# Optimization experiments

Measured on AMD Instinct MI355X. Metric: run time of the kernel, lower is better.

## Reference

```python
import jax, jax.numpy as jnp
import numpy as np

B, S, IN_DIM, OUT_DIM = 4, 2048, 1024, 1024
NEG = -9e15

def _xavier(key, shape, gain=1.414):
    fan_in, fan_out = shape[0], shape[1]
    a = gain * np.sqrt(6.0 / (fan_in + fan_out))
    return jax.random.uniform(key, shape, jnp.float32, -a, a)

def setup_inputs() -> dict:
    key = jax.random.key(0)
    ks = jax.random.split(key, 8)
    x = jax.random.normal(ks[0], (B, S, IN_DIM), jnp.float32)
    W_query = _xavier(ks[1], (IN_DIM, OUT_DIM))
    W_key = _xavier(ks[2], (IN_DIM, OUT_DIM))
    W_value = _xavier(ks[3], (IN_DIM, OUT_DIM))
    # torch Linear default init (kaiming-uniform-ish); values don't matter for correctness baseline
    W1 = _xavier(ks[4], (OUT_DIM + IN_DIM, OUT_DIM), gain=1.0)
    b1 = jnp.zeros((OUT_DIM,), jnp.float32)
    W2 = _xavier(ks[5], (OUT_DIM, OUT_DIM), gain=1.0)
    b2 = jnp.zeros((OUT_DIM,), jnp.float32)
    return {"x": x, "W_query": W_query, "W_key": W_key, "W_value": W_value,
            "W1": W1, "b1": b1, "W2": W2, "b2": b2}

def reference(x, W_query, W_key, W_value, W1, b1, W2, b2):
    # QKV projections: [B,S,in] @ [in,out] -> [B,S,out]
    q = jnp.einsum('bsi,io->bso', x, W_query)
    k = jnp.einsum('bsi,io->bso', x, W_key)
    v = jnp.einsum('bsi,io->bso', x, W_value)
    scale = 1.0 / jnp.sqrt(jnp.float32(OUT_DIM))
    e = jnp.einsum('bqd,bkd->bqk', q, k) * scale  # [B,S,S]
    causal = jnp.tril(jnp.ones((S, S), jnp.float32))  # mask > 0 keeps lower triangle
    attn = jnp.where(causal > 0, e, jnp.float32(NEG))
    attn = jax.nn.softmax(attn, axis=2)
    # dropout: eval mode (train=False) -> identity
    out = jnp.einsum('bqk,bkd->bqd', attn, v)  # [B,S,out]
    h = jnp.concatenate([out, x], axis=-1)  # [B,S,out+in]
    h = jax.nn.relu(jnp.einsum('bsf,fo->bso', h, W1) + b1)
    return jnp.einsum('bsf,fo->bso', h, W2) + b2
```

## Files before the change

kernel.cpp:

```cpp
#include <hip/hip_runtime.h>
#include <stdint.h>

typedef __attribute__((ext_vector_type(8))) short short8;
typedef __attribute__((ext_vector_type(4))) float f32x4;

__device__ __forceinline__ unsigned short f32_to_bf16(float f) {
    unsigned int u = __float_as_uint(f);
    u += 0x7FFFu + ((u >> 16) & 1u);
    return (unsigned short)(u >> 16);
}

__device__ __forceinline__ short8 load8_f32_as_bf16(const float* __restrict__ ap) {
    f32x4 f0 = *(const f32x4*)ap;
    f32x4 f1 = *(const f32x4*)(ap + 4);
    union { short8 s; unsigned short u[8]; } cv;
#pragma unroll
    for (int t = 0; t < 4; ++t) {
        cv.u[t]     = f32_to_bf16(f0[t]);
        cv.u[t + 4] = f32_to_bf16(f1[t]);
    }
    return cv.s;
}

__device__ __forceinline__ void gld_lds16(const void* g, void* l) {
    __builtin_amdgcn_global_load_lds(
        (const __attribute__((address_space(1))) unsigned int*)(unsigned long long)(uintptr_t)g,
        (__attribute__((address_space(3))) unsigned int*)(unsigned int)(uintptr_t)l,
        16, 0, 0);
}

template<int AMODE, int EPI, int SWIZ, bool KLIMIT>
__global__ __launch_bounds__(256, 4)
void gemm128(const unsigned short* __restrict__ A, const unsigned short* __restrict__ A2,
             int lda, int lda2, int ksplit,
             const unsigned short* __restrict__ B, int ldb,
             void* __restrict__ C, int ldc, int K,
             long aStride, long bStride, long cStride,
             const float* __restrict__ bias, long biasStride, float scale)
{
    int z = blockIdx.z;
    int mblk, nblk;
    if (SWIZ == 1) {
        int lin = blockIdx.y * gridDim.x + blockIdx.x;
        int mchunk = gridDim.y >> 3;
        int xcd = lin & 7, idx = lin >> 3;
        mblk = xcd * mchunk + idx % mchunk;
        nblk = idx / mchunk;
    } else if (SWIZ == 2) {
        int x = blockIdx.x;
        int a = (int)((sqrtf(8.f * x + 1.f) - 1.f) * 0.5f);
        while ((a + 1) * (a + 2) / 2 <= x) ++a;
        while (a * (a + 1) / 2 > x) --a;
        mblk = a;
        nblk = x - a * (a + 1) / 2;
    } else if (SWIZ == 3) {
        int lin = blockIdx.y * gridDim.x + blockIdx.x;
        int nchunk = gridDim.x >> 3;
        int xcd = lin & 7, idx = lin >> 3;
        nblk = xcd * nchunk + idx % nchunk;
        mblk = idx / nchunk;
    } else if (SWIZ == 4) {
        mblk = (z & 2) ? ((int)gridDim.y - 1 - (int)blockIdx.y) : blockIdx.y;
        nblk = blockIdx.x;
    } else {
        mblk = blockIdx.y;
        nblk = blockIdx.x;
    }
    int m0 = mblk * 128;
    int n0 = nblk * 128;

    const unsigned short* Ab = A + (size_t)z * aStride;
    const unsigned short* Bb = B + (size_t)z * bStride;

    __shared__ __align__(16) short As[128 * 64];
    __shared__ __align__(16) short Bs[128 * 64];

    int tid  = threadIdx.x;
    int lane = tid & 63, wid = tid >> 6;
    int wm = (wid & 1) * 64, wn = (wid >> 1) * 64;
    int fr = lane & 15, fq = lane >> 4;
    int sw0 = ((fq    ) ^ (fr & 7)) * 16;
    int sw1 = ((fq ^ 4) ^ (fr & 7)) * 16;

    int rS = tid >> 3;
    int cS = ((tid & 7) ^ (rS & 7)) * 8;
    char* AsB = (char*)As; char* BsB = (char*)Bs;

    int kend = KLIMIT ? min(K, m0 + 128) : K;

    f32x4 acc[4][4];
#pragma unroll
    for (int i = 0; i < 4; ++i)
#pragma unroll
    for (int j = 0; j < 4; ++j) acc[i][j] = f32x4{0.f, 0.f, 0.f, 0.f};

    for (int k0 = 0; k0 < kend; k0 += 64) {
        const unsigned short* Asrc = Ab;
        int koff = k0, ldax = lda;
        if (AMODE == 2 && k0 >= ksplit) { Asrc = A2; koff = k0 - ksplit; ldax = lda2; }
        const unsigned short* pa = Asrc + (size_t)(m0 + rS) * ldax + koff + cS;
        const unsigned short* pb = Bb   + (size_t)(n0 + rS) * ldb  + k0   + cS;
#pragma unroll
        for (int t = 0; t < 4; ++t) {
            gld_lds16(pa + (size_t)(32 * t) * ldax, AsB + t * 4096 + tid * 16);
            gld_lds16(pb + (size_t)(32 * t) * ldb,  BsB + t * 4096 + tid * 16);
        }
        __syncthreads();

#pragma unroll
        for (int kh = 0; kh < 2; ++kh) {
            int sw = kh ? sw1 : sw0;
            short8 a[4], b[4];
#pragma unroll
            for (int i = 0; i < 4; ++i) {
                a[i] = *(const short8*)(AsB + (wm + i * 16 + fr) * 128 + sw);
                b[i] = *(const short8*)(BsB + (wn + i * 16 + fr) * 128 + sw);
            }
#pragma unroll
            for (int i = 0; i < 4; ++i)
#pragma unroll
            for (int j = 0; j < 4; ++j)
                acc[i][j] = __builtin_amdgcn_mfma_f32_16x16x32_bf16(a[i], b[j], acc[i][j], 0, 0, 0);
        }
        __syncthreads();
    }

    if (EPI == 6) {
        unsigned short* Cz = (unsigned short*)C + (size_t)z * cStride;
        float* rs = const_cast<float*>(bias) + z * biasStride;
#pragma unroll
        for (int i = 0; i < 4; ++i)
#pragma unroll
        for (int r = 0; r < 4; ++r) {
            int row = m0 + wm + i * 16 + fq * 4 + r;
            float s = 0.f;
#pragma unroll
            for (int j = 0; j < 4; ++j) {
                int col = n0 + wn + j * 16 + fr;
                float e = (col <= row) ? __expf(acc[i][j][r] * scale - 16.f) : 0.f;
                s += e;
                Cz[(size_t)row * ldc + col] = f32_to_bf16(e);
            }
            s += __shfl_xor(s, 1);
            s += __shfl_xor(s, 2);
            s += __shfl_xor(s, 4);
            s += __shfl_xor(s, 8);
            if (fr == 0) atomicAdd(&rs[row], s);
        }
    } else if (EPI == 4) {
        unsigned short* Cz = (unsigned short*)C + (size_t)z * cStride;
#pragma unroll
        for (int i = 0; i < 4; ++i)
#pragma unroll
        for (int r = 0; r < 4; ++r) {
            int row = m0 + wm + i * 16 + fq * 4 + r;
            float inv = 1.f / bias[z * biasStride + row];
#pragma unroll
            for (int j = 0; j < 4; ++j) {
                int col = n0 + wn + j * 16 + fr;
                Cz[(size_t)row * ldc + col] = f32_to_bf16(acc[i][j][r] * inv);
            }
        }
    } else {
#pragma unroll
        for (int i = 0; i < 4; ++i)
#pragma unroll
        for (int j = 0; j < 4; ++j)
#pragma unroll
        for (int r = 0; r < 4; ++r) {
            int row = m0 + wm + i * 16 + fq * 4 + r;
            int col = n0 + wn + j * 16 + fr;
            float v = acc[i][j][r];
            if (EPI == 0) {
                ((unsigned short*)C + (size_t)z * cStride)[(size_t)row * ldc + col] = f32_to_bf16(v);
            } else if (EPI == 2) {
                v += bias[col];
                v = v > 0.f ? v : 0.f;
                ((unsigned short*)C + (size_t)z * cStride)[(size_t)row * ldc + col] = f32_to_bf16(v);
            } else {
                ((float*)C + (size_t)z * cStride)[(size_t)row * ldc + col] = v + bias[col];
            }
        }
    }
}

__device__ __forceinline__ void transpose_tile32(const float* __restrict__ in,
                                                 unsigned short* __restrict__ out,
                                                 int rows, int cols, int bx, int by, int tid)
{
    __shared__ float t[32][33];
    int tx = tid & 31, ty = tid >> 5;
    int r0 = by * 32, c0 = bx * 32;
#pragma unroll
    for (int i = 0; i < 4; ++i)
        t[ty + i * 8][tx] = in[(size_t)(r0 + ty + i * 8) * cols + c0 + tx];
    __syncthreads();
#pragma unroll
    for (int i = 0; i < 4; ++i)
        out[(size_t)(c0 + ty + i * 8) * rows + r0 + tx] = f32_to_bf16(t[tx][ty + i * 8]);
}

__global__ __launch_bounds__(256)
void prep_kernel(const float* __restrict__ x,
                 const float* __restrict__ Wq, const float* __restrict__ Wk,
                 const float* __restrict__ Wv, const float* __restrict__ W1,
                 const float* __restrict__ W2,
                 unsigned short* __restrict__ xb, unsigned short* __restrict__ WT,
                 unsigned short* __restrict__ W1T, unsigned short* __restrict__ W2T,
                 float* __restrict__ rsum)
{
    int idx = blockIdx.x;
    int tid = threadIdx.x;
    if (idx < 4096) {
        size_t i = ((size_t)idx * 256 + tid) * 8;
        *(short8*)(xb + i) = load8_f32_as_bf16(x + i);
    } else if (idx < 7168) {
        int t = idx - 4096;
        int w = t >> 10; t &= 1023;
        const float* in = w == 0 ? Wq : (w == 1 ? Wk : Wv);
        transpose_tile32(in, WT + (size_t)w * 1024 * 1024, 1024, 1024,
                         t & 31, t >> 5, tid);
    } else if (idx < 9216) {
        int t = idx - 7168;
        transpose_tile32(W1, W1T, 2048, 1024, t & 31, t >> 5, tid);
    } else if (idx < 10240) {
        int t = idx - 9216;
        transpose_tile32(W2, W2T, 1024, 1024, t & 31, t >> 5, tid);
    } else {
        int t = idx - 10240;
        f32x4 zero = {0.f, 0.f, 0.f, 0.f};
        float* p = rsum + ((size_t)t * 256 + tid) * 8;
        *(f32x4*)p = zero;
        *(f32x4*)(p + 4) = zero;
    }
}

extern "C" void kernel_launch(void* const* d_in, const int* in_sizes, int n_in,
                              void* d_out, int out_size, void* d_ws, size_t ws_size,
                              hipStream_t stream)
{
    const float* x  = (const float*)d_in[0];
    const float* Wq = (const float*)d_in[1];
    const float* Wk = (const float*)d_in[2];
    const float* Wv = (const float*)d_in[3];
    const float* W1 = (const float*)d_in[4];
    const float* b1 = (const float*)d_in[5];
    const float* W2 = (const float*)d_in[6];
    const float* b2 = (const float*)d_in[7];
    float* out = (float*)d_out;

    size_t off = 0;
    auto alloc = [&](size_t bytes) {
        char* r = (char*)d_ws + off;
        off += (bytes + 255) & ~(size_t)255;
        return r;
    };
    const size_t TOK = (size_t)8192 * 1024;
    unsigned short* WT   = (unsigned short*)alloc((size_t)3072 * 1024 * 2);
    unsigned short* W1T  = (unsigned short*)alloc((size_t)1024 * 2048 * 2);
    unsigned short* W2T  = (unsigned short*)alloc((size_t)1024 * 1024 * 2);
    unsigned short* xb   = (unsigned short*)alloc(TOK * 2);
    unsigned short* vT   = (unsigned short*)alloc((size_t)1024 * 8192 * 2);
    unsigned short* attn = (unsigned short*)alloc(TOK * 2);
    float*          rsum = (float*)         alloc((size_t)4 * 2048 * 4);
    unsigned short* q    = (unsigned short*)alloc(TOK * 2);
    unsigned short* k    = (unsigned short*)alloc(TOK * 2);
    unsigned short* S    = (unsigned short*)alloc((size_t)4 * 2048 * 2048 * 2);
    unsigned short* h1   = S;

    prep_kernel<<<10244, 256, 0, stream>>>(x, Wq, Wk, Wv, W1, W2, xb, WT, W1T, W2T, rsum);

    gemm128<0, 0, 1, false><<<dim3(8, 64, 2), 256, 0, stream>>>(
        xb, nullptr, 1024, 0, 0, WT, 1024, q, 1024, 1024,
        0, (long)1024 * 1024, (long)TOK, nullptr, 0, 0.f);
    gemm128<0, 0, 3, false><<<dim3(64, 8, 1), 256, 0, stream>>>(
        WT + (size_t)2 * 1024 * 1024, nullptr, 1024, 0, 0, xb, 1024, vT, 8192, 1024,
        0, 0, 0, nullptr, 0, 0.f);

    gemm128<0, 6, 2, false><<<dim3(136, 1, 4), 256, 0, stream>>>(
        q, nullptr, 1024, 0, 0, k, 1024, S, 2048, 1024,
        (long)2048 * 1024, (long)2048 * 1024, (long)2048 * 2048, rsum, 2048, 0.03125f);
    gemm128<0, 4, 4, true><<<dim3(8, 16, 4), 256, 0, stream>>>(
        S, nullptr, 2048, 0, 0, vT, 8192, attn, 1024, 2048,
        (long)2048 * 2048, (long)2048, (long)2048 * 1024, rsum, 2048, 0.f);

    gemm128<2, 2, 1, false><<<dim3(8, 64, 1), 256, 0, stream>>>(
        attn, xb, 1024, 1024, 1024, W1T, 2048, h1, 1024, 2048, 0, 0, 0, b1, 0, 0.f);
    gemm128<0, 3, 1, false><<<dim3(8, 64, 1), 256, 0, stream>>>(
        h1, nullptr, 1024, 0, 0, W2T, 1024, out, 1024, 1024, 0, 0, 0, b2, 0, 0.f);
}
```

Before: 301.5 us.

## Use 64-row M tiles, fuse QKV launches, add finer causal tile mapping

Adds an M-tile template parameter and switches the attention, MLP and scores GEMMs to 64x128 tiles, which doubles the block count so more CUs are busy and causal skipping becomes finer grained. The q/k and transposed-v projections are merged into a single launch with a z-dependent operand swap and a second output pointer. A new triangular index mapping for 64-row blocks replaces the old 128x128 one. Smaller tiles lower per-block arithmetic intensity and add global load traffic in exchange for better occupancy and load balance.

New measurement: 299.5 us. No clear change (-0.7%).

```diff
diff --git a/kernel.cpp b/kernel.cpp
--- a/kernel.cpp
+++ b/kernel.cpp
@@ -29,14 +29,20 @@
         16, 0, 0);
 }
 
-template<int AMODE, int EPI, int SWIZ, bool KLIMIT>
+__device__ __forceinline__ int triC(int y) {
+    int t = y >> 1;
+    return y + t * (t - 1) + ((y & 1) ? t : 0);
+}
+
+template<int AMODE, int EPI, int SWIZ, bool KLIMIT, int MT>
 __global__ __launch_bounds__(256, 4)
 void gemm128(const unsigned short* __restrict__ A, const unsigned short* __restrict__ A2,
              int lda, int lda2, int ksplit,
              const unsigned short* __restrict__ B, int ldb,
              void* __restrict__ C, int ldc, int K,
              long aStride, long bStride, long cStride,
-             const float* __restrict__ bias, long biasStride, float scale)
+             const float* __restrict__ bias, long biasStride, float scale,
+             void* __restrict__ C2, int ldc2)
 {
     int z = blockIdx.z;
     int mblk, nblk;
@@ -46,38 +52,45 @@
         int xcd = lin & 7, idx = lin >> 3;
         mblk = xcd * mchunk + idx % mchunk;
         nblk = idx / mchunk;
-    } else if (SWIZ == 2) {
-        int x = blockIdx.x;
-        int a = (int)((sqrtf(8.f * x + 1.f) - 1.f) * 0.5f);
-        while ((a + 1) * (a + 2) / 2 <= x) ++a;
-        while (a * (a + 1) / 2 > x) --a;
-        mblk = a;
-        nblk = x - a * (a + 1) / 2;
-    } else if (SWIZ == 3) {
-        int lin = blockIdx.y * gridDim.x + blockIdx.x;
-        int nchunk = gridDim.x >> 3;
-        int xcd = lin & 7, idx = lin >> 3;
-        nblk = xcd * nchunk + idx % nchunk;
-        mblk = idx / nchunk;
     } else if (SWIZ == 4) {
         mblk = (z & 2) ? ((int)gridDim.y - 1 - (int)blockIdx.y) : blockIdx.y;
         nblk = blockIdx.x;
+    } else if (SWIZ == 5) {
+        int x = blockIdx.x;
+        int a = (int)(2.f * sqrtf((float)x));
+        if (a > 31) a = 31;
+        while (a < 31 && triC(a + 1) <= x) ++a;
+        while (a > 0 && triC(a) > x) --a;
+        mblk = a;
+        nblk = x - triC(a);
+    } else if (SWIZ == 6) {
+        int x = blockIdx.x, yy = blockIdx.y;
+        if (z < 2) { mblk = x * 8 + (yy & 7); nblk = yy >> 3; }
+        else       { nblk = x * 8 + (yy & 7); mblk = yy >> 3; }
     } else {
         mblk = blockIdx.y;
         nblk = blockIdx.x;
     }
-    int m0 = mblk * 128;
+    int m0 = mblk * MT;
     int n0 = nblk * 128;
 
-    const unsigned short* Ab = A + (size_t)z * aStride;
-    const unsigned short* Bb = B + (size_t)z * bStride;
-
-    __shared__ __align__(16) short As[128 * 64];
+    const unsigned short* Ab;
+    const unsigned short* Bb;
+    if (SWIZ == 6) {
+        if (z < 2) { Ab = A; Bb = B + (size_t)z * bStride; }
+        else       { Ab = B + (size_t)2 * bStride; Bb = A; }
+    } else {
+        Ab = A + (size_t)z * aStride;
+        Bb = B + (size_t)z * bStride;
+    }
+
+    __shared__ __align__(16) short As[MT * 64];
     __shared__ __align__(16) short Bs[128 * 64];
 
     int tid  = threadIdx.x;
     int lane = tid & 63, wid = tid >> 6;
-    int wm = (wid & 1) * 64, wn = (wid >> 1) * 64;
+    constexpr int MI = MT / 32;
+    int wm = (wid & 1) * (MT / 2), wn = (wid >> 1) * 64;
     int fr = lane & 15, fq = lane >> 4;
     int sw0 = ((fq    ) ^ (fr & 7)) * 16;
     int sw1 = ((fq ^ 4) ^ (fr & 7)) * 16;
@@ -86,11 +99,11 @@
     int cS = ((tid & 7) ^ (rS & 7)) * 8;
     char* AsB = (char*)As; char* BsB = (char*)Bs;
 
-    int kend = KLIMIT ? min(K, m0 + 128) : K;
-
-    f32x4 acc[4][4];
-#pragma unroll
-    for (int i = 0; i < 4; ++i)
+    int kend = KLIMIT ? min(K, m0 + MT) : K;
+
+    f32x4 acc[MI][4];
+#pragma unroll
+    for (int i = 0; i < MI; ++i)
 #pragma unroll
     for (int j = 0; j < 4; ++j) acc[i][j] = f32x4{0.f, 0.f, 0.f, 0.f};
 
@@ -101,23 +114,25 @@
         const unsigned short* pa = Asrc + (size_t)(m0 + rS) * ldax + koff + cS;
         const unsigned short* pb = Bb   + (size_t)(n0 + rS) * ldb  + k0   + cS;
 #pragma unroll
-        for (int t = 0; t < 4; ++t) {
+        for (int t = 0; t < MT / 32; ++t)
             gld_lds16(pa + (size_t)(32 * t) * ldax, AsB + t * 4096 + tid * 16);
+#pragma unroll
+        for (int t = 0; t < 4; ++t)
             gld_lds16(pb + (size_t)(32 * t) * ldb,  BsB + t * 4096 + tid * 16);
-        }
         __syncthreads();
 
 #pragma unroll
         for (int kh = 0; kh < 2; ++kh) {
             int sw = kh ? sw1 : sw0;
-            short8 a[4], b[4];
-#pragma unroll
-            for (int i = 0; i < 4; ++i) {
+            short8 a[MI], b[4];
+#pragma unroll
+            for (int i = 0; i < MI; ++i)
                 a[i] = *(const short8*)(AsB + (wm + i * 16 + fr) * 128 + sw);
-                b[i] = *(const short8*)(BsB + (wn + i * 16 + fr) * 128 + sw);
-            }
-#pragma unroll
-            for (int i = 0; i < 4; ++i)
+#pragma unroll
+            for (int j = 0; j < 4; ++j)
+                b[j] = *(const short8*)(BsB + (wn + j * 16 + fr) * 128 + sw);
+#pragma unroll
+            for (int i = 0; i < MI; ++i)
 #pragma unroll
             for (int j = 0; j < 4; ++j)
                 acc[i][j] = __builtin_amdgcn_mfma_f32_16x16x32_bf16(a[i], b[j], acc[i][j], 0, 0, 0);
@@ -125,11 +140,25 @@
         __syncthreads();
     }
 
-    if (EPI == 6) {
+    if (EPI == 0) {
+        unsigned short* Cz; int ldcz;
+        if (SWIZ == 6 && z >= 2) { Cz = (unsigned short*)C2; ldcz = ldc2; }
+        else { Cz = (unsigned short*)C + (size_t)z * cStride; ldcz = ldc; }
+#pragma unroll
+        for (int i = 0; i < MI; ++i)
+#pragma unroll
+        for (int j = 0; j < 4; ++j)
+#pragma unroll
+        for (int r = 0; r < 4; ++r) {
+            int row = m0 + wm + i * 16 + fq * 4 + r;
+            int col = n0 + wn + j * 16 + fr;
+            Cz[(size_t)row * ldcz + col] = f32_to_bf16(acc[i][j][r]);
+        }
+    } else if (EPI == 6) {
         unsigned short* Cz = (unsigned short*)C + (size_t)z * cStride;
         float* rs = const_cast<float*>(bias) + z * biasStride;
 #pragma unroll
-        for (int i = 0; i < 4; ++i)
+        for (int i = 0; i < MI; ++i)
 #pragma unroll
         for (int r = 0; r < 4; ++r) {
             int row = m0 + wm + i * 16 + fq * 4 + r;
@@ -150,7 +179,7 @@
     } else if (EPI == 4) {
         unsigned short* Cz = (unsigned short*)C + (size_t)z * cStride;
 #pragma unroll
-        for (int i = 0; i < 4; ++i)
+        for (int i = 0; i < MI; ++i)
 #pragma unroll
         for (int r = 0; r < 4; ++r) {
             int row = m0 + wm + i * 16 + fq * 4 + r;
@@ -163,7 +192,7 @@
         }
     } else {
 #pragma unroll
-        for (int i = 0; i < 4; ++i)
+        for (int i = 0; i < MI; ++i)
 #pragma unroll
         for (int j = 0; j < 4; ++j)
 #pragma unroll
@@ -171,9 +200,7 @@
             int row = m0 + wm + i * 16 + fq * 4 + r;
             int col = n0 + wn + j * 16 + fr;
             float v = acc[i][j][r];
-            if (EPI == 0) {
-                ((unsigned short*)C + (size_t)z * cStride)[(size_t)row * ldc + col] = f32_to_bf16(v);
-            } else if (EPI == 2) {
+            if (EPI == 2) {
                 v += bias[col];
                 v = v > 0.f ? v : 0.f;
                 ((unsigned short*)C + (size_t)z * cStride)[(size_t)row * ldc + col] = f32_to_bf16(v);
@@ -270,22 +297,22 @@
 
     prep_kernel<<<10244, 256, 0, stream>>>(x, Wq, Wk, Wv, W1, W2, xb, WT, W1T, W2T, rsum);
 
-    gemm128<0, 0, 1, false><<<dim3(8, 64, 2), 256, 0, stream>>>(
+    gemm128<0, 0, 6, false, 128><<<dim3(8, 64, 3), 256, 0, stream>>>(
         xb, nullptr, 1024, 0, 0, WT, 1024, q, 1024, 1024,
-        0, (long)1024 * 1024, (long)TOK, nullptr, 0, 0.f);
-    gemm128<0, 0, 3, false><<<dim3(64, 8, 1), 256, 0, stream>>>(
-        WT + (size_t)2 * 1024 * 1024, nullptr, 1024, 0, 0, xb, 1024, vT, 8192, 1024,
-        0, 0, 0, nullptr, 0, 0.f);
-
-    gemm128<0, 6, 2, false><<<dim3(136, 1, 4), 256, 0, stream>>>(
+        0, (long)1024 * 1024, (long)TOK, nullptr, 0, 0.f, vT, 8192);
+
+    gemm128<0, 6, 5, false, 64><<<dim3(272, 1, 4), 256, 0, stream>>>(
         q, nullptr, 1024, 0, 0, k, 1024, S, 2048, 1024,
-        (long)2048 * 1024, (long)2048 * 1024, (long)2048 * 2048, rsum, 2048, 0.03125f);
-    gemm128<0, 4, 4, true><<<dim3(8, 16, 4), 256, 0, stream>>>(
+        (long)2048 * 1024, (long)2048 * 1024, (long)2048 * 2048, rsum, 2048, 0.03125f,
+        nullptr, 0);
+    gemm128<0, 4, 4, true, 64><<<dim3(8, 32, 4), 256, 0, stream>>>(
         S, nullptr, 2048, 0, 0, vT, 8192, attn, 1024, 2048,
-        (long)2048 * 2048, (long)2048, (long)2048 * 1024, rsum, 2048, 0.f);
-
-    gemm128<2, 2, 1, false><<<dim3(8, 64, 1), 256, 0, stream>>>(
-        attn, xb, 1024, 1024, 1024, W1T, 2048, h1, 1024, 2048, 0, 0, 0, b1, 0, 0.f);
-    gemm128<0, 3, 1, false><<<dim3(8, 64, 1), 256, 0, stream>>>(
-        h1, nullptr, 1024, 0, 0, W2T, 1024, out, 1024, 1024, 0, 0, 0, b2, 0, 0.f);
-}
+        (long)2048 * 2048, (long)2048, (long)2048 * 1024, rsum, 2048, 0.f, nullptr, 0);
+
+    gemm128<2, 2, 1, false, 64><<<dim3(8, 128, 1), 256, 0, stream>>>(
+        attn, xb, 1024, 1024, 1024, W1T, 2048, h1, 1024, 2048, 0, 0, 0, b1, 0, 0.f,
+        nullptr, 0);
+    gemm128<0, 3, 1, false, 64><<<dim3(8, 128, 1), 256, 0, stream>>>(
+        h1, nullptr, 1024, 0, 0, W2T, 1024, out, 1024, 1024, 0, 0, 0, b2, 0, 0.f,
+        nullptr, 0);
+}
```
